# Kernel tuning notes

Measured on AMD Instinct MI355X. Metric: run time of the kernel, lower is better.

The kernel has to match this reference:

```python
import jax, jax.numpy as jnp
import numpy as np

BITS = 4
NPACK = 32 // BITS            # 8 nibbles per int32
GROUPSIZE = 128
IN_F = 8192
OUT_F = 8192
BATCH = 64
NGROUPS = IN_F // GROUPSIZE   # 64
MASK = (1 << BITS) - 1        # 15


def setup_inputs() -> dict:
    key = jax.random.key(0)
    k1, k2, k3, k4, k5 = jax.random.split(key, 5)
    x = jax.random.normal(k1, (BATCH, IN_F), dtype=jnp.float32)
    qweight = jax.random.randint(k2, (IN_F // NPACK, OUT_F), 0, 2**31 - 1, dtype=jnp.int32)
    qzeros = jax.random.randint(k3, (NGROUPS, OUT_F // NPACK), 0, 2**31 - 1, dtype=jnp.int32)
    scales = jax.random.uniform(k4, (NGROUPS, OUT_F), dtype=jnp.float32, minval=1e-3, maxval=1e-2)
    bias = jax.random.normal(k5, (OUT_F,), dtype=jnp.float32)
    return {"x": x, "qweight": qweight, "qzeros": qzeros, "scales": scales, "bias": bias}


def _dequantize(qweight, qzeros, scales):
    shifts = (jnp.arange(NPACK, dtype=jnp.int32) * BITS)
    # unpack weight nibbles along in_features: [in/8, 8, out] -> [in, out]
    w = (qweight[:, None, :] >> shifts[None, :, None]) & MASK
    w = w.reshape(IN_F, OUT_F).astype(jnp.float32)
    # unpack zero points along out_features: [g, out/8, 8] -> [g, out]
    zp = (qzeros[:, :, None] >> shifts[None, None, :]) & MASK
    zp = zp.reshape(NGROUPS, OUT_F) + 1                       # optimum format stores zp-1
    zp = jnp.where(zp > MASK, 0, zp).astype(jnp.float32)      # wraparound per recover()
    g_idx = jnp.arange(IN_F) // GROUPSIZE                     # per-input-channel group id
    return (w - zp[g_idx]) * scales[g_idx]                    # [in, out] fp weight


def reference(x, qweight, qzeros, scales, bias):
    W = _dequantize(qweight, qzeros, scales)                  # [in, out]
    return x @ W + bias                                       # F.linear(x, W.T, bias)
```

## Files before the change

### kernel.cpp

```cpp
#include <hip/hip_runtime.h>
#include <hip/hip_bf16.h>

#define IN_F 8192
#define OUT_F 8192
#define BATCH 64
#define KSPLIT 8

typedef __attribute__((ext_vector_type(8))) _Float16 f16x8_t;
typedef __attribute__((ext_vector_type(2))) _Float16 f16x2_t;
typedef __attribute__((ext_vector_type(8))) ushort   u16x8_t;
typedef __attribute__((ext_vector_type(4))) float    f32x4_t;

__global__ void __launch_bounds__(512, 4)
wol_mfma(const float*  __restrict__ x,
         const int*    __restrict__ qw,
         const int*    __restrict__ qz,
         const float*  __restrict__ sc,
         ushort*       __restrict__ part) {
    const int nt   = blockIdx.x & 31;
    const int ks   = blockIdx.x >> 5;
    const int wid  = threadIdx.x >> 6;
    const int lane = threadIdx.x & 63;
    const int ln   = lane & 15;
    const int kb   = lane >> 4;
    const int colbase = nt * 256 + wid * 32;
    const int k0      = ks * 1024;
    const int gbase   = k0 >> 7;
    const int qrowb   = k0 >> 3;

    unsigned qc[4][2]; float svc[2]; unsigned zwc[2];
#pragma unroll
    for (int kt = 0; kt < 4; ++kt)
#pragma unroll
        for (int nj = 0; nj < 2; ++nj)
            qc[kt][nj] = (unsigned)qw[(size_t)(qrowb + kt * 4 + kb) * OUT_F +
                                      colbase + nj * 16 + ln];
#pragma unroll
    for (int nj = 0; nj < 2; ++nj) {
        const int c = colbase + nj * 16 + ln;
        svc[nj] = sc[gbase * OUT_F + c];
        zwc[nj] = (unsigned)qz[gbase * (OUT_F / 8) + (c >> 3)];
    }
    __builtin_amdgcn_sched_barrier(0);

    __shared__ ushort lds_x[128 * 64 * 8];
    {
        const int perm[8] = {0, 4, 1, 5, 2, 6, 3, 7};
#pragma unroll
        for (int i = 0; i < 16; ++i) {
            const int idx = i * 512 + (int)threadIdx.x;
            const int row = idx >> 7;
            const int k8l = idx & 127;
            const float4* sp = (const float4*)&x[(size_t)row * IN_F + k0 + k8l * 8];
            const float4 a = sp[0], b = sp[1];
            const float f[8] = {a.x, a.y, a.z, a.w, b.x, b.y, b.z, b.w};
            union { ushort u[8]; u16x8_t v; } o;
#pragma unroll
            for (int j = 0; j < 8; ++j) {
                const _Float16 h = (_Float16)f[perm[j]];
                o.u[j] = *(const ushort*)&h;
            }
            unsigned byteoff = (unsigned)(row * 2048 + k8l * 16);
            byteoff ^= (unsigned)((row & 7) << 4);
            *(u16x8_t*)((char*)lds_x + byteoff) = o.v;
        }
    }
    __syncthreads();

    const unsigned xorv = (unsigned)((ln & 7) << 4);

    f32x4_t acc[4][2];
#pragma unroll
    for (int mi = 0; mi < 4; ++mi)
#pragma unroll
        for (int nj = 0; nj < 2; ++nj) acc[mi][nj] = (f32x4_t)0.0f;

#pragma unroll 1
    for (int g = 0; g < 8; ++g) {
        unsigned qn[4][2]; float svn[2]; unsigned zwn[2];
        if (g < 7) {
            const int qrow1 = qrowb + (g + 1) * 16;
#pragma unroll
            for (int kt = 0; kt < 4; ++kt)
#pragma unroll
                for (int nj = 0; nj < 2; ++nj)
                    qn[kt][nj] = (unsigned)qw[(size_t)(qrow1 + kt * 4 + kb) * OUT_F +
                                              colbase + nj * 16 + ln];
#pragma unroll
            for (int nj = 0; nj < 2; ++nj) {
                const int c = colbase + nj * 16 + ln;
                svn[nj] = sc[(gbase + g + 1) * OUT_F + c];
                zwn[nj] = (unsigned)qz[(gbase + g + 1) * (OUT_F / 8) + (c >> 3)];
            }
            __builtin_amdgcn_sched_barrier(0);
        }

        f16x2_t c2[2], s2[2];
#pragma unroll
        for (int nj = 0; nj < 2; ++nj) {
            const unsigned zp = ((zwc[nj] >> ((ln & 7) * 4)) + 1u) & 15u;
            const _Float16 hc = (_Float16)(-(float)(1024u + zp));
            const _Float16 hs = (_Float16)svc[nj];
            c2[nj][0] = hc; c2[nj][1] = hc;
            s2[nj][0] = hs; s2[nj][1] = hs;
        }

#pragma unroll
        for (int kt = 0; kt < 4; ++kt) {
            const unsigned kbyte = (unsigned)(g * 256 + kt * 64 + kb * 16) ^ xorv;
            f16x8_t af[4];
#pragma unroll
            for (int mi = 0; mi < 4; ++mi)
                af[mi] = *(const f16x8_t*)((const char*)lds_x +
                            (unsigned)((mi * 16 + ln) * 2048) + kbyte);
#pragma unroll
            for (int nj = 0; nj < 2; ++nj) {
                const unsigned qv = qc[kt][nj];
                const unsigned r0 = ( qv        & 0x000F000Fu) | 0x64006400u;
                const unsigned r1 = ((qv >> 4)  & 0x000F000Fu) | 0x64006400u;
                const unsigned r2 = ((qv >> 8)  & 0x000F000Fu) | 0x64006400u;
                const unsigned r3 = ((qv >> 12) & 0x000F000Fu) | 0x64006400u;
                union { unsigned u[4]; f16x8_t v; } bu;
                union { unsigned u; f16x2_t h; } t0, t1, t2, t3;
                t0.u = r0; t1.u = r1; t2.u = r2; t3.u = r3;
                f16x2_t w0 = (t0.h + c2[nj]) * s2[nj];
                f16x2_t w1 = (t1.h + c2[nj]) * s2[nj];
                f16x2_t w2 = (t2.h + c2[nj]) * s2[nj];
                f16x2_t w3 = (t3.h + c2[nj]) * s2[nj];
                bu.u[0] = *(const unsigned*)&w0;
                bu.u[1] = *(const unsigned*)&w1;
                bu.u[2] = *(const unsigned*)&w2;
                bu.u[3] = *(const unsigned*)&w3;
#pragma unroll
                for (int mi = 0; mi < 4; ++mi)
                    acc[mi][nj] = __builtin_amdgcn_mfma_f32_16x16x32_f16(
                        af[mi], bu.v, acc[mi][nj], 0, 0, 0);
            }
        }

        if (g < 7) {
#pragma unroll
            for (int kt = 0; kt < 4; ++kt)
#pragma unroll
                for (int nj = 0; nj < 2; ++nj) qc[kt][nj] = qn[kt][nj];
#pragma unroll
            for (int nj = 0; nj < 2; ++nj) { svc[nj] = svn[nj]; zwc[nj] = zwn[nj]; }
        }
    }

    union { ushort u[32]; u16x8_t v8[4]; } ob;
#pragma unroll
    for (int mi = 0; mi < 4; ++mi)
#pragma unroll
        for (int nj = 0; nj < 2; ++nj)
#pragma unroll
            for (int j = 0; j < 4; ++j) {
                __hip_bfloat16 h = __float2bfloat16(acc[mi][nj][j]);
                ob.u[(mi * 2 + nj) * 4 + j] = *reinterpret_cast<ushort*>(&h);
            }
    u16x8_t* pb = (u16x8_t*)part + ((size_t)(ks * 32 + nt) * 512 + threadIdx.x) * 4;
#pragma unroll
    for (int i = 0; i < 4; ++i) pb[i] = ob.v8[i];
}

__global__ void __launch_bounds__(256)
wol_reduce(const ushort* __restrict__ part,
           const float*  __restrict__ bias,
           float* __restrict__ out) {
    const int u   = blockIdx.x * 256 + threadIdx.x;
    const int v8  = u & 3;
    const int tid = (u >> 2) & 511;
    const int nt  = u >> 11;

    float s[8];
#pragma unroll
    for (int e = 0; e < 8; ++e) s[e] = 0.0f;
#pragma unroll
    for (int ks = 0; ks < KSPLIT; ++ks) {
        const u16x8_t p = *((const u16x8_t*)part +
                            (((size_t)(ks * 32 + nt) * 512 + tid) * 4 + v8));
#pragma unroll
        for (int e = 0; e < 8; ++e) {
            union { unsigned b; float f; } cv;
            cv.b = ((unsigned)(ushort)p[e]) << 16;
            s[e] += cv.f;
        }
    }

    const int wid = tid >> 6, lane = tid & 63;
    const int ln = lane & 15, kb = lane >> 4;
#pragma unroll
    for (int e = 0; e < 8; ++e) {
        const int idx = v8 * 8 + e;
        const int mi = idx >> 3, nj = (idx >> 2) & 1, j = idx & 3;
        const int row = mi * 16 + kb * 4 + j;
        const int col = nt * 256 + wid * 32 + nj * 16 + ln;
        out[(size_t)row * OUT_F + col] = s[e] + bias[col];
    }
}

extern "C" void kernel_launch(void* const* d_in, const int* in_sizes, int n_in,
                              void* d_out, int out_size, void* d_ws, size_t ws_size,
                              hipStream_t stream) {
    const float* x    = (const float*)d_in[0];
    const int*   qw   = (const int*)d_in[1];
    const int*   qz   = (const int*)d_in[2];
    const float* sc   = (const float*)d_in[3];
    const float* bias = (const float*)d_in[4];
    float* out = (float*)d_out;

    ushort* prt = (ushort*)d_ws;

    (void)in_sizes; (void)n_in; (void)ws_size; (void)out_size;

    wol_mfma<<<256, 512, 0, stream>>>(x, qw, qz, sc, prt);
    wol_reduce<<<256, 256, 0, stream>>>(prt, bias, out);
}
```

Measured before the change: 25.28 us.

## Fuse split-K GEMM and reduction into one cooperative kernel with grid sync

Merges the MFMA partial-product kernel and the split-K reduction kernel into a single cooperative launch separated by a grid-wide barrier. Each thread then reduces four bf16 partials across the eight K-slices and adds the bias. The aim is to remove the second kernel launch and its inter-kernel gap. The cost is a grid-sync barrier and cooperative-launch overhead, and the occupancy hint drops from 4 to 2 blocks per CU.

```diff
diff --git a/kernel.cpp b/kernel.cpp
--- a/kernel.cpp
+++ b/kernel.cpp
@@ -1,5 +1,8 @@
 #include <hip/hip_runtime.h>
 #include <hip/hip_bf16.h>
+#include <hip/hip_cooperative_groups.h>
+
+namespace cg = cooperative_groups;
 
 #define IN_F 8192
 #define OUT_F 8192
@@ -9,14 +12,17 @@
 typedef __attribute__((ext_vector_type(8))) _Float16 f16x8_t;
 typedef __attribute__((ext_vector_type(2))) _Float16 f16x2_t;
 typedef __attribute__((ext_vector_type(8))) ushort   u16x8_t;
+typedef __attribute__((ext_vector_type(4))) ushort   u16x4_t;
 typedef __attribute__((ext_vector_type(4))) float    f32x4_t;
 
-__global__ void __launch_bounds__(512, 4)
-wol_mfma(const float*  __restrict__ x,
-         const int*    __restrict__ qw,
-         const int*    __restrict__ qz,
-         const float*  __restrict__ sc,
-         ushort*       __restrict__ part) {
+__global__ void __launch_bounds__(512, 2)
+wol_fused(const float*  __restrict__ x,
+          const int*    __restrict__ qw,
+          const int*    __restrict__ qz,
+          const float*  __restrict__ sc,
+          ushort*       __restrict__ part,
+          const float*  __restrict__ bias,
+          float*        __restrict__ out) {
     const int nt   = blockIdx.x & 31;
     const int ks   = blockIdx.x >> 5;
     const int wid  = threadIdx.x >> 6;
@@ -161,41 +167,36 @@
     u16x8_t* pb = (u16x8_t*)part + ((size_t)(ks * 32 + nt) * 512 + threadIdx.x) * 4;
 #pragma unroll
     for (int i = 0; i < 4; ++i) pb[i] = ob.v8[i];
-}
-
-__global__ void __launch_bounds__(256)
-wol_reduce(const ushort* __restrict__ part,
-           const float*  __restrict__ bias,
-           float* __restrict__ out) {
-    const int u   = blockIdx.x * 256 + threadIdx.x;
-    const int v8  = u & 3;
-    const int tid = (u >> 2) & 511;
-    const int nt  = u >> 11;
-
-    float s[8];
-#pragma unroll
-    for (int e = 0; e < 8; ++e) s[e] = 0.0f;
-#pragma unroll
-    for (int ks = 0; ks < KSPLIT; ++ks) {
-        const u16x8_t p = *((const u16x8_t*)part +
-                            (((size_t)(ks * 32 + nt) * 512 + tid) * 4 + v8));
-#pragma unroll
-        for (int e = 0; e < 8; ++e) {
+
+    cg::this_grid().sync();
+
+    const int u    = blockIdx.x * 512 + (int)threadIdx.x;
+    const int v4   = u & 7;
+    const int tidA = (u >> 3) & 511;
+    const int ntR  = u >> 12;
+
+    float s4[4] = {0.0f, 0.0f, 0.0f, 0.0f};
+#pragma unroll
+    for (int k2 = 0; k2 < KSPLIT; ++k2) {
+        const u16x4_t p = *((const u16x4_t*)part +
+                            (((size_t)(k2 * 32 + ntR) * 512 + tidA) * 8 + v4));
+#pragma unroll
+        for (int e = 0; e < 4; ++e) {
             union { unsigned b; float f; } cv;
             cv.b = ((unsigned)(ushort)p[e]) << 16;
-            s[e] += cv.f;
-        }
-    }
-
-    const int wid = tid >> 6, lane = tid & 63;
-    const int ln = lane & 15, kb = lane >> 4;
-#pragma unroll
-    for (int e = 0; e < 8; ++e) {
-        const int idx = v8 * 8 + e;
+            s4[e] += cv.f;
+        }
+    }
+
+    const int widR = tidA >> 6, laneR = tidA & 63;
+    const int lnR = laneR & 15, kbR = laneR >> 4;
+#pragma unroll
+    for (int e = 0; e < 4; ++e) {
+        const int idx = v4 * 4 + e;
         const int mi = idx >> 3, nj = (idx >> 2) & 1, j = idx & 3;
-        const int row = mi * 16 + kb * 4 + j;
-        const int col = nt * 256 + wid * 32 + nj * 16 + ln;
-        out[(size_t)row * OUT_F + col] = s[e] + bias[col];
+        const int row = mi * 16 + kbR * 4 + j;
+        const int col = ntR * 256 + widR * 32 + nj * 16 + lnR;
+        out[(size_t)row * OUT_F + col] = s4[e] + bias[col];
     }
 }
 
@@ -213,6 +214,8 @@
 
     (void)in_sizes; (void)n_in; (void)ws_size; (void)out_size;
 
-    wol_mfma<<<256, 512, 0, stream>>>(x, qw, qz, sc, prt);
-    wol_reduce<<<256, 256, 0, stream>>>(prt, bias, out);
+    void* args[] = {(void*)&x, (void*)&qw, (void*)&qz, (void*)&sc,
+                    (void*)&prt, (void*)&bias, (void*)&out};
+    hipLaunchCooperativeKernel((void*)wol_fused, dim3(256), dim3(512),
+                               args, 0, stream);
 }
```

Result: slower. 74.81 us (+196.0%).
